# Kernel tuning notes

Measured on AMD Instinct MI355X. Metric: run time of the kernel, lower is better.

## Reference

```python
import jax, jax.numpy as jnp
import numpy as np

B, L, V, H = 64, 2048, 1024, 256
HALF = H // 2


def setup_inputs() -> dict:
    key = jax.random.key(0)
    ks = jax.random.split(key, 8)
    s = lambda k, shape, scale=0.05: jax.random.normal(k, shape, jnp.float32) * scale
    return {
        "seq": jax.random.randint(ks[0], (B, L), 0, V),
        "embed": s(ks[1], (V, H)),
        "w1": s(ks[2], (H, 2 * H)), "b1": jnp.zeros((2 * H,), jnp.float32),
        "w2": s(ks[3], (2 * H, H)), "b2": jnp.zeros((H,), jnp.float32),
        "ln_g": jnp.ones((H,), jnp.float32), "ln_b": jnp.zeros((H,), jnp.float32),
        "kp_w": s(ks[4], (H, H)), "kp_b": jnp.zeros((H,), jnp.float32),
        "out_w": s(ks[5], (H, V)), "out_b": jnp.zeros((V,), jnp.float32),
    }


def _forward(seq, embed, w1, b1, w2, b2, ln_g, ln_b, kp_w, kp_b, out_w, out_b):
    # Encoder: embed -> FFN residual -> LayerNorm
    e = embed[seq]                                    # [B, L, H]
    ff = jax.nn.relu(e @ w1 + b1) @ w2 + b2           # [B, L, H]
    x = e + ff
    mu = x.mean(-1, keepdims=True)
    var = jnp.mean((x - mu) ** 2, -1, keepdims=True)
    h = (x - mu) * jax.lax.rsqrt(var + 1e-5) * ln_g + ln_b

    # Shared key projection for all timesteps at once
    proj = h @ kp_w + kp_b                            # [B, L, H]
    ks_all = proj[:, : L - 1, :HALF]                  # [B, L-1, half]
    ke_all = proj[:, : L - 1, HALF:]                  # [B, L-1, half]
    scale = (jnp.arange(L - 1, dtype=jnp.float32) + 1.0) / L  # (t+1)/L

    def step(carry, inp):
        M_s, M_e = carry
        k_s, k_e, sc = inp                            # [B,half], [B,half], scalar
        vps = jnp.einsum('bij,bj->bi', M_s, k_s)
        dvs = k_s - vps / (jnp.sum(k_s * k_s, -1, keepdims=True) + 1e-6)
        M_s = M_s + jnp.einsum('bi,bj->bij', dvs, k_s)
        vpe = jnp.einsum('bij,bj->bi', M_e, k_e)
        dve = k_e - vpe / (jnp.sum(k_e * k_e, -1, keepdims=True) + 1e-6)
        M_e = M_e + sc * jnp.einsum('bi,bj->bij', dve, k_e)
        return (M_s, M_e), None

    M0 = jnp.zeros((B, HALF, HALF), jnp.float32)
    (M_s, M_e), _ = jax.lax.scan(
        step, (M0, M0),
        (ks_all.transpose(1, 0, 2), ke_all.transpose(1, 0, 2), scale))

    q = proj[:, -1, :]                                # query from last step
    cs = jnp.einsum('bij,bj->bi', M_s, q[:, :HALF])
    ce = jnp.einsum('bij,bj->bi', M_e, q[:, HALF:])
    return jnp.concatenate([cs, ce], -1) @ out_w + out_b  # [B, V]


def reference(seq, embed, w1, b1, w2, b2, ln_g, ln_b, kp_w, kp_b, out_w, out_b):
    return _forward(seq, embed, w1, b1, w2, b2, ln_g, ln_b, kp_w, kp_b, out_w, out_b)
```

## Files before the change

kernel.cpp:

```cpp
#include <hip/hip_runtime.h>
#include <hip/hip_bf16.h>
#include <stdint.h>

#define B_SZ 64
#define L_SZ 2048
#define V_SZ 1024
#define H_SZ 256
#define HALF_SZ 128
#define NTOK (B_SZ * L_SZ)
#define CH 16384

typedef unsigned short ushort_t;
typedef __attribute__((ext_vector_type(8))) short bf16x8;
typedef __attribute__((ext_vector_type(4))) float f32x4;

__device__ __forceinline__ ushort_t f2bf(float f) {
    __hip_bfloat16 h = __float2bfloat16(f);
    return *reinterpret_cast<ushort_t*>(&h);
}

__global__ __launch_bounds__(256) void cvt_bf16_k(
    const float* __restrict__ src, ushort_t* __restrict__ dst, int n)
{
    int i = (blockIdx.x * 256 + threadIdx.x) * 4;
    if (i >= n) return;
    float4 v = *(const float4*)(src + i);
    uint2 pk;
    pk.x = (uint32_t)f2bf(v.x) | ((uint32_t)f2bf(v.y) << 16);
    pk.y = (uint32_t)f2bf(v.z) | ((uint32_t)f2bf(v.w) << 16);
    *(uint2*)(dst + i) = pk;
}

__global__ __launch_bounds__(256) void transpose_cvt_k(
    const float* __restrict__ src, ushort_t* __restrict__ dst, int K, int N)
{
    int idx = blockIdx.x * 256 + threadIdx.x;
    if (idx >= K * N) return;
    int n = idx / K;
    int k = idx - n * K;
    dst[idx] = f2bf(src[(size_t)k * N + n]);
}

template <int MODE, int K, int N>
__global__ __launch_bounds__(256) void gemm_mfma(
    const ushort_t* __restrict__ A, const ushort_t* __restrict__ BT,
    const float* __restrict__ bias, void* __restrict__ Cp,
    const int* __restrict__ seq, const float* __restrict__ embed)
{
    __shared__ __align__(16) ushort_t Asm[128 * 64];
    __shared__ __align__(16) ushort_t Bsm[128 * 64];

    const int tid = threadIdx.x;
    const int m0 = blockIdx.x * 128;
    const int n0 = blockIdx.y * 128;
    const int w = tid >> 6;
    const int l = tid & 63;
    const int wr = w >> 1;
    const int wc = w & 1;

    const ushort_t* arow[4];
    const ushort_t* brow[4];
#pragma unroll
    for (int i = 0; i < 4; ++i) {
        const int flat = i * 256 + tid;
        const int r = flat >> 3;
        const int gr = (MODE == 1) ? seq[m0 + r] : (m0 + r);
        arow[i] = A + (size_t)gr * K;
        brow[i] = BT + (size_t)(n0 + r) * K;
    }

    f32x4 acc[4][4];
#pragma unroll
    for (int mi = 0; mi < 4; ++mi)
#pragma unroll
        for (int nj = 0; nj < 4; ++nj)
            acc[mi][nj] = (f32x4){0.f, 0.f, 0.f, 0.f};

    for (int kt = 0; kt < K / 64; ++kt) {
#pragma unroll
        for (int i = 0; i < 4; ++i) {
            const int flat = i * 256 + tid;
            const int r = flat >> 3;
            const int c = flat & 7;
            const int cs = c ^ (r & 7);
            uint4 av = *(const uint4*)(arow[i] + kt * 64 + c * 8);
            *(uint4*)&Asm[r * 64 + cs * 8] = av;
            uint4 bv = *(const uint4*)(brow[i] + kt * 64 + c * 8);
            *(uint4*)&Bsm[r * 64 + cs * 8] = bv;
        }
        __syncthreads();
#pragma unroll
        for (int kh = 0; kh < 2; ++kh) {
            bf16x8 af[4], bfr[4];
#pragma unroll
            for (int mi = 0; mi < 4; ++mi) {
                const int r = wr * 64 + mi * 16 + (l & 15);
                const int c = (kh * 4 + (l >> 4)) ^ (r & 7);
                af[mi] = *(const bf16x8*)&Asm[r * 64 + c * 8];
            }
#pragma unroll
            for (int nj = 0; nj < 4; ++nj) {
                const int r = wc * 64 + nj * 16 + (l & 15);
                const int c = (kh * 4 + (l >> 4)) ^ (r & 7);
                bfr[nj] = *(const bf16x8*)&Bsm[r * 64 + c * 8];
            }
#pragma unroll
            for (int mi = 0; mi < 4; ++mi)
#pragma unroll
                for (int nj = 0; nj < 4; ++nj)
                    acc[mi][nj] = __builtin_amdgcn_mfma_f32_16x16x32_bf16(
                        af[mi], bfr[nj], acc[mi][nj], 0, 0, 0);
        }
        __syncthreads();
    }

    const int cl = l & 15;
    const int rg = l >> 4;
    float bv[4];
#pragma unroll
    for (int nj = 0; nj < 4; ++nj)
        bv[nj] = bias[n0 + wc * 64 + nj * 16 + cl];

#pragma unroll
    for (int mi = 0; mi < 4; ++mi) {
#pragma unroll
        for (int i = 0; i < 4; ++i) {
            const int row = m0 + wr * 64 + mi * 16 + rg * 4 + i;
            const float* erow = (MODE == 2)
                ? (embed + (size_t)seq[row] * H_SZ) : nullptr;
#pragma unroll
            for (int nj = 0; nj < 4; ++nj) {
                const int gn = n0 + wc * 64 + nj * 16 + cl;
                float v = acc[mi][nj][i] + bv[nj];
                if (MODE == 1) {
                    v = fmaxf(v, 0.f);
                    ((ushort_t*)Cp)[(size_t)row * N + gn] = f2bf(v);
                } else if (MODE == 2) {
                    ((float*)Cp)[(size_t)row * N + gn] = v + erow[gn];
                } else {
                    ((float*)Cp)[(size_t)row * N + gn] = v;
                }
            }
        }
    }
}

__global__ __launch_bounds__(256) void ln_k(
    const float* __restrict__ x, const float* __restrict__ g,
    const float* __restrict__ bt, ushort_t* __restrict__ h)
{
    const int token = blockIdx.x * 4 + (threadIdx.x >> 6);
    const int lane = threadIdx.x & 63;
    const float* xr = x + (size_t)token * H_SZ + lane * 4;
    const float4 v = *(const float4*)xr;
    float s = v.x + v.y + v.z + v.w;
    float sq = v.x * v.x + v.y * v.y + v.z * v.z + v.w * v.w;
#pragma unroll
    for (int m = 1; m < 64; m <<= 1) {
        s += __shfl_xor(s, m);
        sq += __shfl_xor(sq, m);
    }
    const float mu = s * (1.f / H_SZ);
    const float var = sq * (1.f / H_SZ) - mu * mu;
    const float rs = rsqrtf(var + 1e-5f);
    const int idx = lane * 4;
    const float4 gg = *(const float4*)(g + idx);
    const float4 bb = *(const float4*)(bt + idx);
    ushort_t o0 = f2bf((v.x - mu) * rs * gg.x + bb.x);
    ushort_t o1 = f2bf((v.y - mu) * rs * gg.y + bb.y);
    ushort_t o2 = f2bf((v.z - mu) * rs * gg.z + bb.z);
    ushort_t o3 = f2bf((v.w - mu) * rs * gg.w + bb.w);
    uint2 pk;
    pk.x = (uint32_t)o0 | ((uint32_t)o1 << 16);
    pk.y = (uint32_t)o2 | ((uint32_t)o3 << 16);
    *(uint2*)(h + (size_t)token * H_SZ + idx) = pk;
}

__global__ __launch_bounds__(256) void invn_k(
    const float* __restrict__ proj, float* __restrict__ invn)
{
    const int token = blockIdx.x * 4 + (threadIdx.x >> 6);
    const int lane = threadIdx.x & 63;
    const float4 v = *(const float4*)(proj + (size_t)token * H_SZ + lane * 4);
    float sq = v.x * v.x + v.y * v.y + v.z * v.z + v.w * v.w;
#pragma unroll
    for (int m = 1; m < 32; m <<= 1) sq += __shfl_xor(sq, m);
    if ((lane & 31) == 0)
        invn[(size_t)token * 2 + (lane >> 5)] = 1.0f / (sq + 1e-6f);
}

__global__ __launch_bounds__(64) void scan_bw_k(
    const float* __restrict__ proj, const float* __restrict__ invn,
    float* __restrict__ cbuf)
{
    const int pair = blockIdx.x;
    const int b = pair >> 1;
    const int half = pair & 1;
    const int l = threadIdx.x;

    const float* kbase = proj + (size_t)b * L_SZ * H_SZ + half * HALF_SZ;
    const float* ibase = invn + (size_t)b * L_SZ * 2 + half;
    const float invL = 1.0f / (float)L_SZ;

    float2 v = *(const float2*)(kbase + (size_t)(L_SZ - 1) * H_SZ + 2 * l);
    float2 c = make_float2(0.f, 0.f);

    float2 kc[4], kn[4];
    float inc_[4], inn_[4];
#pragma unroll
    for (int i = 0; i < 4; ++i) {
        kc[i] = *(const float2*)(kbase + (size_t)(2046 - i) * H_SZ + 2 * l);
        inc_[i] = ibase[(size_t)(2046 - i) * 2];
        kn[i] = *(const float2*)(kbase + (size_t)(2042 - i) * H_SZ + 2 * l);
        inn_[i] = ibase[(size_t)(2042 - i) * 2];
    }

    for (int tb = 2046; tb >= 6; tb -= 4) {
        float2 kf[4];
        float inf_[4];
#pragma unroll
        for (int i = 0; i < 4; ++i) {
            int tp = tb - 8 - i;
            tp = tp < 0 ? 0 : tp;
            kf[i] = *(const float2*)(kbase + (size_t)tp * H_SZ + 2 * l);
            inf_[i] = ibase[(size_t)tp * 2];
        }

        float r[10];
        r[0] = kc[0].x * v.x + kc[0].y * v.y;
        r[1] = kc[1].x * v.x + kc[1].y * v.y;
        r[2] = kc[2].x * v.x + kc[2].y * v.y;
        r[3] = kc[3].x * v.x + kc[3].y * v.y;
        r[4] = kc[0].x * kc[1].x + kc[0].y * kc[1].y;
        r[5] = kc[0].x * kc[2].x + kc[0].y * kc[2].y;
        r[6] = kc[0].x * kc[3].x + kc[0].y * kc[3].y;
        r[7] = kc[1].x * kc[2].x + kc[1].y * kc[2].y;
        r[8] = kc[1].x * kc[3].x + kc[1].y * kc[3].y;
        r[9] = kc[2].x * kc[3].x + kc[2].y * kc[3].y;

#pragma unroll
        for (int m = 1; m < 64; m <<= 1) {
#pragma unroll
            for (int j = 0; j < 10; ++j) r[j] += __shfl_xor(r[j], m);
        }

        float be[4], al[4];
#pragma unroll
        for (int i = 0; i < 4; ++i) {
            be[i] = half ? (float)(tb - i + 1) * invL : 1.0f;
            al[i] = be[i] * inc_[i];
        }
        const float d0 = r[0];
        const float d1 = r[1] - al[0] * r[4] * d0;
        const float d2 = r[2] - al[0] * r[5] * d0 - al[1] * r[7] * d1;
        const float d3 = r[3] - al[0] * r[6] * d0 - al[1] * r[8] * d1
                              - al[2] * r[9] * d2;

        const float ad0 = al[0] * d0, ad1 = al[1] * d1,
                    ad2 = al[2] * d2, ad3 = al[3] * d3;
        const float bd0 = be[0] * d0, bd1 = be[1] * d1,
                    bd2 = be[2] * d2, bd3 = be[3] * d3;

        v.x -= ad0 * kc[0].x + ad1 * kc[1].x + ad2 * kc[2].x + ad3 * kc[3].x;
        v.y -= ad0 * kc[0].y + ad1 * kc[1].y + ad2 * kc[2].y + ad3 * kc[3].y;
        c.x += bd0 * kc[0].x + bd1 * kc[1].x + bd2 * kc[2].x + bd3 * kc[3].x;
        c.y += bd0 * kc[0].y + bd1 * kc[1].y + bd2 * kc[2].y + bd3 * kc[3].y;

#pragma unroll
        for (int i = 0; i < 4; ++i) {
            kc[i] = kn[i]; inc_[i] = inn_[i];
            kn[i] = kf[i]; inn_[i] = inf_[i];
        }
    }

#pragma unroll
    for (int i = 0; i < 3; ++i) {
        const int t = 2 - i;
        float a = kc[i].x * v.x + kc[i].y * v.y;
#pragma unroll
        for (int m = 1; m < 64; m <<= 1) a += __shfl_xor(a, m);
        const float be = half ? (float)(t + 1) * invL : 1.0f;
        const float al = be * inc_[i];
        const float ad = al * a, bd = be * a;
        v.x -= ad * kc[i].x; v.y -= ad * kc[i].y;
        c.x += bd * kc[i].x; c.y += bd * kc[i].y;
    }

    *(float2*)(cbuf + b * H_SZ + half * HALF_SZ + 2 * l) = c;
}

__global__ __launch_bounds__(256) void out_k(
    const float* __restrict__ c, const float* __restrict__ w,
    const float* __restrict__ ob, float* __restrict__ out)
{
    const int b = blockIdx.x >> 2;
    const int v = ((blockIdx.x & 3) << 8) + threadIdx.x;
    const float* cb = c + b * H_SZ;
    float acc = ob[v];
#pragma unroll 4
    for (int hh = 0; hh < H_SZ; ++hh)
        acc = fmaf(cb[hh], w[(size_t)hh * V_SZ + v], acc);
    out[(size_t)b * V_SZ + v] = acc;
}

extern "C" void kernel_launch(void* const* d_in, const int* in_sizes, int n_in,
                              void* d_out, int out_size, void* d_ws, size_t ws_size,
                              hipStream_t stream)
{
    const int*   seq   = (const int*)d_in[0];
    const float* embed = (const float*)d_in[1];
    const float* w1    = (const float*)d_in[2];
    const float* b1    = (const float*)d_in[3];
    const float* w2    = (const float*)d_in[4];
    const float* b2    = (const float*)d_in[5];
    const float* ln_g  = (const float*)d_in[6];
    const float* ln_b  = (const float*)d_in[7];
    const float* kp_w  = (const float*)d_in[8];
    const float* kp_b  = (const float*)d_in[9];
    const float* out_w = (const float*)d_in[10];
    const float* out_b = (const float*)d_in[11];

    char* ws = (char*)d_ws;
    size_t off = 0;
    auto alloc = [&](size_t bytes) -> void* {
        void* p = ws + off;
        off += (bytes + 255) & ~(size_t)255;
        return p;
    };

    float*    proj = (float*)alloc((size_t)NTOK * H_SZ * sizeof(float));
    ushort_t* t1_c = (ushort_t*)alloc((size_t)CH * 512 * sizeof(ushort_t));
    float*    x_c  = (float*)alloc((size_t)CH * H_SZ * sizeof(float));
    ushort_t* h_c  = (ushort_t*)alloc((size_t)CH * H_SZ * sizeof(ushort_t));
    float*    invn = (float*)alloc((size_t)NTOK * 2 * sizeof(float));
    float*    cbuf = (float*)alloc((size_t)B_SZ * H_SZ * sizeof(float));
    ushort_t* embed_bf = (ushort_t*)alloc((size_t)V_SZ * H_SZ * 2);
    ushort_t* w1T = (ushort_t*)alloc((size_t)512 * 256 * 2);
    ushort_t* w2T = (ushort_t*)alloc((size_t)256 * 512 * 2);
    ushort_t* kpT = (ushort_t*)alloc((size_t)256 * 256 * 2);
    float*    outp = (float*)d_out;

    const dim3 blk(256);

    cvt_bf16_k<<<dim3((V_SZ * H_SZ) / 1024), blk, 0, stream>>>(
        embed, embed_bf, V_SZ * H_SZ);
    transpose_cvt_k<<<dim3((256 * 512) / 256), blk, 0, stream>>>(w1, w1T, 256, 512);
    transpose_cvt_k<<<dim3((512 * 256) / 256), blk, 0, stream>>>(w2, w2T, 512, 256);
    transpose_cvt_k<<<dim3((256 * 256) / 256), blk, 0, stream>>>(kp_w, kpT, 256, 256);

    for (int c = 0; c < NTOK / CH; ++c) {
        const int base = c * CH;
        const int* seq_c = seq + base;
        gemm_mfma<1, 256, 512><<<dim3(CH / 128, 4), blk, 0, stream>>>(
            embed_bf, w1T, b1, t1_c, seq_c, nullptr);
        gemm_mfma<2, 512, 256><<<dim3(CH / 128, 2), blk, 0, stream>>>(
            t1_c, w2T, b2, x_c, seq_c, embed);
        ln_k<<<dim3(CH / 4), blk, 0, stream>>>(x_c, ln_g, ln_b, h_c);
        gemm_mfma<3, 256, 256><<<dim3(CH / 128, 2), blk, 0, stream>>>(
            h_c, kpT, kp_b, proj + (size_t)base * H_SZ, seq_c, nullptr);
    }

    invn_k<<<dim3(NTOK / 4), blk, 0, stream>>>(proj, invn);
    scan_bw_k<<<dim3(128), dim3(64), 0, stream>>>(proj, invn, cbuf);
    out_k<<<dim3(B_SZ * 4), blk, 0, stream>>>(cbuf, out_w, out_b, outp);
}
```

Before: 799.6 us.

## Replace serial backward scan with chunked Gram-matrix solve using split-bf16 MFMA

Replaces the per-step backward scan (one 64-lane wave per batch-half, 4 steps per iteration with shuffle reductions) with a chunked algorithm. Each 128-token chunk goes into LDS as split hi/lo bf16, and a 128x128 Gram matrix is built with three-pass MFMA for near-fp32 accuracy. A triangular forward substitution then produces all per-step coefficients, and v and c are updated in bulk. Key norms are computed in the same kernel, so the separate invn kernel and its buffer are removed. The serial per-token dependency chain shrinks to a 128-step LDS substitution per chunk, at the cost of extra MFMA work, heavy LDS use (about 100KB per block) and only 128 blocks.

```diff
diff --git a/kernel.cpp b/kernel.cpp
--- a/kernel.cpp
+++ b/kernel.cpp
@@ -176,117 +176,193 @@
     *(uint2*)(h + (size_t)token * H_SZ + idx) = pk;
 }
 
-__global__ __launch_bounds__(256) void invn_k(
-    const float* __restrict__ proj, float* __restrict__ invn)
-{
-    const int token = blockIdx.x * 4 + (threadIdx.x >> 6);
-    const int lane = threadIdx.x & 63;
-    const float4 v = *(const float4*)(proj + (size_t)token * H_SZ + lane * 4);
-    float sq = v.x * v.x + v.y * v.y + v.z * v.z + v.w * v.w;
-#pragma unroll
-    for (int m = 1; m < 32; m <<= 1) sq += __shfl_xor(sq, m);
-    if ((lane & 31) == 0)
-        invn[(size_t)token * 2 + (lane >> 5)] = 1.0f / (sq + 1e-6f);
-}
-
-__global__ __launch_bounds__(64) void scan_bw_k(
-    const float* __restrict__ proj, const float* __restrict__ invn,
-    float* __restrict__ cbuf)
-{
+__global__ __launch_bounds__(256) void scan_chunk_k(
+    const float* __restrict__ proj, float* __restrict__ cbuf)
+{
+    __shared__ __align__(16) ushort_t Khi[128 * 128];
+    __shared__ __align__(16) ushort_t Klo[128 * 128];
+    __shared__ __align__(16) float G[128 * 128];
+    __shared__ float vv[128], cc[128], aa[128];
+    __shared__ float al[128], be[128], ad[128], bd[128];
+    __shared__ float pv[2][128], pc[2][128];
+
     const int pair = blockIdx.x;
     const int b = pair >> 1;
     const int half = pair & 1;
-    const int l = threadIdx.x;
+    const int tid = threadIdx.x;
+    const int w = tid >> 6;
+    const int l = tid & 63;
 
     const float* kbase = proj + (size_t)b * L_SZ * H_SZ + half * HALF_SZ;
-    const float* ibase = invn + (size_t)b * L_SZ * 2 + half;
     const float invL = 1.0f / (float)L_SZ;
 
-    float2 v = *(const float2*)(kbase + (size_t)(L_SZ - 1) * H_SZ + 2 * l);
-    float2 c = make_float2(0.f, 0.f);
-
-    float2 kc[4], kn[4];
-    float inc_[4], inn_[4];
-#pragma unroll
-    for (int i = 0; i < 4; ++i) {
-        kc[i] = *(const float2*)(kbase + (size_t)(2046 - i) * H_SZ + 2 * l);
-        inc_[i] = ibase[(size_t)(2046 - i) * 2];
-        kn[i] = *(const float2*)(kbase + (size_t)(2042 - i) * H_SZ + 2 * l);
-        inn_[i] = ibase[(size_t)(2042 - i) * 2];
-    }
-
-    for (int tb = 2046; tb >= 6; tb -= 4) {
-        float2 kf[4];
-        float inf_[4];
-#pragma unroll
-        for (int i = 0; i < 4; ++i) {
-            int tp = tb - 8 - i;
-            tp = tp < 0 ? 0 : tp;
-            kf[i] = *(const float2*)(kbase + (size_t)tp * H_SZ + 2 * l);
-            inf_[i] = ibase[(size_t)tp * 2];
-        }
-
-        float r[10];
-        r[0] = kc[0].x * v.x + kc[0].y * v.y;
-        r[1] = kc[1].x * v.x + kc[1].y * v.y;
-        r[2] = kc[2].x * v.x + kc[2].y * v.y;
-        r[3] = kc[3].x * v.x + kc[3].y * v.y;
-        r[4] = kc[0].x * kc[1].x + kc[0].y * kc[1].y;
-        r[5] = kc[0].x * kc[2].x + kc[0].y * kc[2].y;
-        r[6] = kc[0].x * kc[3].x + kc[0].y * kc[3].y;
-        r[7] = kc[1].x * kc[2].x + kc[1].y * kc[2].y;
-        r[8] = kc[1].x * kc[3].x + kc[1].y * kc[3].y;
-        r[9] = kc[2].x * kc[3].x + kc[2].y * kc[3].y;
-
-#pragma unroll
-        for (int m = 1; m < 64; m <<= 1) {
-#pragma unroll
-            for (int j = 0; j < 10; ++j) r[j] += __shfl_xor(r[j], m);
-        }
-
-        float be[4], al[4];
-#pragma unroll
-        for (int i = 0; i < 4; ++i) {
-            be[i] = half ? (float)(tb - i + 1) * invL : 1.0f;
-            al[i] = be[i] * inc_[i];
-        }
-        const float d0 = r[0];
-        const float d1 = r[1] - al[0] * r[4] * d0;
-        const float d2 = r[2] - al[0] * r[5] * d0 - al[1] * r[7] * d1;
-        const float d3 = r[3] - al[0] * r[6] * d0 - al[1] * r[8] * d1
-                              - al[2] * r[9] * d2;
-
-        const float ad0 = al[0] * d0, ad1 = al[1] * d1,
-                    ad2 = al[2] * d2, ad3 = al[3] * d3;
-        const float bd0 = be[0] * d0, bd1 = be[1] * d1,
-                    bd2 = be[2] * d2, bd3 = be[3] * d3;
-
-        v.x -= ad0 * kc[0].x + ad1 * kc[1].x + ad2 * kc[2].x + ad3 * kc[3].x;
-        v.y -= ad0 * kc[0].y + ad1 * kc[1].y + ad2 * kc[2].y + ad3 * kc[3].y;
-        c.x += bd0 * kc[0].x + bd1 * kc[1].x + bd2 * kc[2].x + bd3 * kc[3].x;
-        c.y += bd0 * kc[0].y + bd1 * kc[1].y + bd2 * kc[2].y + bd3 * kc[3].y;
-
-#pragma unroll
-        for (int i = 0; i < 4; ++i) {
-            kc[i] = kn[i]; inc_[i] = inn_[i];
-            kn[i] = kf[i]; inn_[i] = inf_[i];
-        }
-    }
-
-#pragma unroll
-    for (int i = 0; i < 3; ++i) {
-        const int t = 2 - i;
-        float a = kc[i].x * v.x + kc[i].y * v.y;
-#pragma unroll
-        for (int m = 1; m < 64; m <<= 1) a += __shfl_xor(a, m);
-        const float be = half ? (float)(t + 1) * invL : 1.0f;
-        const float al = be * inc_[i];
-        const float ad = al * a, bd = be * a;
-        v.x -= ad * kc[i].x; v.y -= ad * kc[i].y;
-        c.x += bd * kc[i].x; c.y += bd * kc[i].y;
-    }
-
-    *(float2*)(cbuf + b * H_SZ + half * HALF_SZ + 2 * l) = c;
+    if (tid < 128) {
+        vv[tid] = kbase[(size_t)(L_SZ - 1) * H_SZ + tid];
+        cc[tid] = 0.f;
+    }
+    __syncthreads();
+
+    for (int chk = 15; chk >= 0; --chk) {
+        const int t1 = chk * 128 + 127;
+
+        {
+            const int u = tid >> 1, h = tid & 1;
+            const int tok = t1 - u;
+            const float* src = kbase + (size_t)tok * H_SZ + h * 64;
+            float sq = 0.f;
+#pragma unroll
+            for (int g = 0; g < 8; ++g) {
+                const float4 v0 = *(const float4*)(src + g * 8);
+                const float4 v1 = *(const float4*)(src + g * 8 + 4);
+                const float e[8] = {v0.x, v0.y, v0.z, v0.w,
+                                    v1.x, v1.y, v1.z, v1.w};
+                ushort_t hi8[8], lo8[8];
+#pragma unroll
+                for (int q = 0; q < 8; ++q) {
+                    sq = fmaf(e[q], e[q], sq);
+                    hi8[q] = f2bf(e[q]);
+                    const float hf = __uint_as_float(((uint32_t)hi8[q]) << 16);
+                    lo8[q] = f2bf(e[q] - hf);
+                }
+                const int cs = (h * 8 + g) ^ (u & 7);
+                uint4 ph, pl;
+                ph.x = (uint32_t)hi8[0] | ((uint32_t)hi8[1] << 16);
+                ph.y = (uint32_t)hi8[2] | ((uint32_t)hi8[3] << 16);
+                ph.z = (uint32_t)hi8[4] | ((uint32_t)hi8[5] << 16);
+                ph.w = (uint32_t)hi8[6] | ((uint32_t)hi8[7] << 16);
+                pl.x = (uint32_t)lo8[0] | ((uint32_t)lo8[1] << 16);
+                pl.y = (uint32_t)lo8[2] | ((uint32_t)lo8[3] << 16);
+                pl.z = (uint32_t)lo8[4] | ((uint32_t)lo8[5] << 16);
+                pl.w = (uint32_t)lo8[6] | ((uint32_t)lo8[7] << 16);
+                *(uint4*)&Khi[u * 128 + cs * 8] = ph;
+                *(uint4*)&Klo[u * 128 + cs * 8] = pl;
+            }
+            sq += __shfl_xor(sq, 1);
+            if (h == 0) {
+                float bet, alp;
+                if (tok == L_SZ - 1) { bet = 0.f; alp = 0.f; }
+                else {
+                    bet = half ? (float)(tok + 1) * invL : 1.0f;
+                    alp = bet / (sq + 1e-6f);
+                }
+                al[u] = alp; be[u] = bet;
+            }
+        }
+        __syncthreads();
+
+        {
+#pragma unroll
+            for (int tr = 0; tr < 2; ++tr) {
+                const int ti = 2 * w + tr;
+                const int ra = ti * 16 + (l & 15);
+                bf16x8 ahi[4], alo[4];
+#pragma unroll
+                for (int ks = 0; ks < 4; ++ks) {
+                    const int c = (ks * 4 + (l >> 4)) ^ (ra & 7);
+                    ahi[ks] = *(const bf16x8*)&Khi[ra * 128 + c * 8];
+                    alo[ks] = *(const bf16x8*)&Klo[ra * 128 + c * 8];
+                }
+#pragma unroll
+                for (int tj = 0; tj < 8; ++tj) {
+                    const int rb = tj * 16 + (l & 15);
+                    f32x4 acc = (f32x4){0.f, 0.f, 0.f, 0.f};
+#pragma unroll
+                    for (int ks = 0; ks < 4; ++ks) {
+                        const int c = (ks * 4 + (l >> 4)) ^ (rb & 7);
+                        const bf16x8 bhi = *(const bf16x8*)&Khi[rb * 128 + c * 8];
+                        const bf16x8 blo = *(const bf16x8*)&Klo[rb * 128 + c * 8];
+                        acc = __builtin_amdgcn_mfma_f32_16x16x32_bf16(
+                            ahi[ks], bhi, acc, 0, 0, 0);
+                        acc = __builtin_amdgcn_mfma_f32_16x16x32_bf16(
+                            ahi[ks], blo, acc, 0, 0, 0);
+                        acc = __builtin_amdgcn_mfma_f32_16x16x32_bf16(
+                            alo[ks], bhi, acc, 0, 0, 0);
+                    }
+                    const int col = tj * 16 + (l & 15);
+                    const int rbase = ti * 16 + (l >> 4) * 4;
+#pragma unroll
+                    for (int i = 0; i < 4; ++i)
+                        G[(rbase + i) * 128 + col] = acc[i];
+                }
+            }
+        }
+
+        {
+            const int u = tid >> 1, h = tid & 1;
+            float p = 0.f;
+#pragma unroll
+            for (int g = 0; g < 8; ++g) {
+                const int cs = (h * 8 + g) ^ (u & 7);
+                const uint4 ph = *(const uint4*)&Khi[u * 128 + cs * 8];
+                const uint4 pl = *(const uint4*)&Klo[u * 128 + cs * 8];
+                const float* vp = &vv[(h * 8 + g) * 8];
+                const float4 w0 = *(const float4*)vp;
+                const float4 w1 = *(const float4*)(vp + 4);
+                const uint32_t Hh[4] = {ph.x, ph.y, ph.z, ph.w};
+                const uint32_t Ll[4] = {pl.x, pl.y, pl.z, pl.w};
+                const float wv[8] = {w0.x, w0.y, w0.z, w0.w,
+                                     w1.x, w1.y, w1.z, w1.w};
+#pragma unroll
+                for (int q = 0; q < 4; ++q) {
+                    const float k0 = __uint_as_float(Hh[q] << 16)
+                                   + __uint_as_float(Ll[q] << 16);
+                    const float k1 = __uint_as_float(Hh[q] & 0xffff0000u)
+                                   + __uint_as_float(Ll[q] & 0xffff0000u);
+                    p = fmaf(k0, wv[2 * q], p);
+                    p = fmaf(k1, wv[2 * q + 1], p);
+                }
+            }
+            p += __shfl_xor(p, 1);
+            if (h == 0) aa[u] = p;
+        }
+        __syncthreads();
+
+        {
+            float acc0 = aa[l];
+            float acc1 = aa[l + 64];
+#pragma unroll 8
+            for (int j = 0; j < 128; ++j) {
+                const float cur = (j < 64) ? acc0 : acc1;
+                const float db = __shfl(cur, j & 63);
+                const float adj = al[j] * db;
+                const float g0 = G[j * 128 + l];
+                const float g1 = G[j * 128 + l + 64];
+                acc0 -= ((l > j) ? adj : 0.f) * g0;
+                acc1 -= ((l + 64 > j) ? adj : 0.f) * g1;
+                if (w == 0 && l == (j & 63)) {
+                    ad[j] = adj;
+                    bd[j] = be[j] * db;
+                }
+            }
+        }
+        __syncthreads();
+
+        {
+            const int g = tid >> 7;
+            const int e = tid & 127;
+            const int ch0 = e >> 3, o = e & 7;
+            float pvv = 0.f, pcc = 0.f;
+#pragma unroll 8
+            for (int j = g * 64; j < g * 64 + 64; ++j) {
+                const int idx = j * 128 + ((ch0 ^ (j & 7)) << 3) + o;
+                const float k = __uint_as_float(((uint32_t)Khi[idx]) << 16)
+                              + __uint_as_float(((uint32_t)Klo[idx]) << 16);
+                pvv = fmaf(ad[j], k, pvv);
+                pcc = fmaf(bd[j], k, pcc);
+            }
+            pv[g][e] = pvv; pc[g][e] = pcc;
+        }
+        __syncthreads();
+
+        if (tid < 128) {
+            vv[tid] -= pv[0][tid] + pv[1][tid];
+            cc[tid] += pc[0][tid] + pc[1][tid];
+        }
+        __syncthreads();
+    }
+
+    if (tid < 128)
+        cbuf[b * H_SZ + half * HALF_SZ + tid] = cc[tid];
 }
 
 __global__ __launch_bounds__(256) void out_k(
@@ -332,7 +408,6 @@
     ushort_t* t1_c = (ushort_t*)alloc((size_t)CH * 512 * sizeof(ushort_t));
     float*    x_c  = (float*)alloc((size_t)CH * H_SZ * sizeof(float));
     ushort_t* h_c  = (ushort_t*)alloc((size_t)CH * H_SZ * sizeof(ushort_t));
-    float*    invn = (float*)alloc((size_t)NTOK * 2 * sizeof(float));
     float*    cbuf = (float*)alloc((size_t)B_SZ * H_SZ * sizeof(float));
     ushort_t* embed_bf = (ushort_t*)alloc((size_t)V_SZ * H_SZ * 2);
     ushort_t* w1T = (ushort_t*)alloc((size_t)512 * 256 * 2);
@@ -360,7 +435,6 @@
             h_c, kpT, kp_b, proj + (size_t)base * H_SZ, seq_c, nullptr);
     }
 
-    invn_k<<<dim3(NTOK / 4), blk, 0, stream>>>(proj, invn);
-    scan_bw_k<<<dim3(128), dim3(64), 0, stream>>>(proj, invn, cbuf);
+    scan_chunk_k<<<dim3(128), blk, 0, stream>>>(proj, cbuf);
     out_k<<<dim3(B_SZ * 4), blk, 0, stream>>>(cbuf, out_w, out_b, outp);
 }
```

Measured after the change: 824.8 us. +3.1%, slower.

## Precompute blocked Gram coefficients in parallel; scan backward in blocks of eight

Applied to the files above, without the earlier changes.

Moves the key-key Gram products and inverse-norm scaling out of the sequential backward scan into a parallel pre-pass that writes per-block coefficient sets of eight tokens. The scan then does only eight query dot products per step with one batched wave reduction and a small triangular solve, halving the number of serial steps. This cuts reductions on the latency-bound critical path of the 128-wave scan, at the cost of an extra kernel, a coefficient buffer, and higher register pressure in the scan.

```diff
diff --git a/kernel.cpp b/kernel.cpp
--- a/kernel.cpp
+++ b/kernel.cpp
@@ -176,21 +176,68 @@
     *(uint2*)(h + (size_t)token * H_SZ + idx) = pk;
 }
 
-__global__ __launch_bounds__(256) void invn_k(
-    const float* __restrict__ proj, float* __restrict__ invn)
-{
-    const int token = blockIdx.x * 4 + (threadIdx.x >> 6);
-    const int lane = threadIdx.x & 63;
-    const float4 v = *(const float4*)(proj + (size_t)token * H_SZ + lane * 4);
-    float sq = v.x * v.x + v.y * v.y + v.z * v.z + v.w * v.w;
-#pragma unroll
-    for (int m = 1; m < 32; m <<= 1) sq += __shfl_xor(sq, m);
-    if ((lane & 31) == 0)
-        invn[(size_t)token * 2 + (lane >> 5)] = 1.0f / (sq + 1e-6f);
-}
-
-__global__ __launch_bounds__(64) void scan_bw_k(
-    const float* __restrict__ proj, const float* __restrict__ invn,
+__global__ __launch_bounds__(256) void gram8_k(
+    const float* __restrict__ proj, float* __restrict__ g8)
+{
+    const int pair = blockIdx.y;
+    const int b = pair >> 1;
+    const int half = pair & 1;
+    const int bi = blockIdx.x * 4 + (threadIdx.x >> 6);
+    const int l = threadIdx.x & 63;
+
+    const float* kbase = proj + (size_t)b * L_SZ * H_SZ + half * HALF_SZ;
+
+    float2 kk[8];
+#pragma unroll
+    for (int i = 0; i < 8; ++i) {
+        const int tok = bi * 8 + 7 - i;
+        kk[i] = *(const float2*)(kbase + (size_t)tok * H_SZ + 2 * l);
+    }
+
+    float r[36];
+#pragma unroll
+    for (int i = 0; i < 8; ++i)
+        r[i] = kk[i].x * kk[i].x + kk[i].y * kk[i].y;
+#pragma unroll
+    for (int i = 1; i < 8; ++i)
+#pragma unroll
+        for (int j = 0; j < i; ++j)
+            r[8 + i * (i - 1) / 2 + j] = kk[i].x * kk[j].x + kk[i].y * kk[j].y;
+
+#pragma unroll
+    for (int m = 1; m < 64; m <<= 1)
+#pragma unroll
+        for (int t = 0; t < 36; ++t)
+            r[t] += __shfl_xor(r[t], m);
+
+    const float invL = 1.0f / (float)L_SZ;
+    float al[8], be[8];
+#pragma unroll
+    for (int i = 0; i < 8; ++i) {
+        const int tok = bi * 8 + 7 - i;
+        const float bet = (tok == L_SZ - 1)
+            ? 0.f : (half ? (float)(tok + 1) * invL : 1.0f);
+        be[i] = bet;
+        al[i] = bet / (r[i] + 1e-6f);
+    }
+
+    if (l == 0) {
+        float* out = g8 + ((size_t)pair * 256 + bi) * 48;
+#pragma unroll
+        for (int i = 1; i < 8; ++i)
+#pragma unroll
+            for (int j = 0; j < i; ++j)
+                out[i * (i - 1) / 2 + j] = al[j] * r[8 + i * (i - 1) / 2 + j];
+#pragma unroll
+        for (int i = 0; i < 8; ++i) {
+            out[28 + i] = al[i];
+            out[36 + i] = be[i];
+        }
+    }
+}
+
+__global__ __launch_bounds__(64) void scan_bw8_k(
+    const float* __restrict__ proj, const float* __restrict__ g8,
     float* __restrict__ cbuf)
 {
     const int pair = blockIdx.x;
@@ -199,91 +246,77 @@
     const int l = threadIdx.x;
 
     const float* kbase = proj + (size_t)b * L_SZ * H_SZ + half * HALF_SZ;
-    const float* ibase = invn + (size_t)b * L_SZ * 2 + half;
-    const float invL = 1.0f / (float)L_SZ;
+    const float* gbase = g8 + (size_t)pair * 256 * 48;
 
     float2 v = *(const float2*)(kbase + (size_t)(L_SZ - 1) * H_SZ + 2 * l);
     float2 c = make_float2(0.f, 0.f);
 
-    float2 kc[4], kn[4];
-    float inc_[4], inn_[4];
-#pragma unroll
-    for (int i = 0; i < 4; ++i) {
-        kc[i] = *(const float2*)(kbase + (size_t)(2046 - i) * H_SZ + 2 * l);
-        inc_[i] = ibase[(size_t)(2046 - i) * 2];
-        kn[i] = *(const float2*)(kbase + (size_t)(2042 - i) * H_SZ + 2 * l);
-        inn_[i] = ibase[(size_t)(2042 - i) * 2];
-    }
-
-    for (int tb = 2046; tb >= 6; tb -= 4) {
-        float2 kf[4];
-        float inf_[4];
-#pragma unroll
-        for (int i = 0; i < 4; ++i) {
-            int tp = tb - 8 - i;
-            tp = tp < 0 ? 0 : tp;
-            kf[i] = *(const float2*)(kbase + (size_t)tp * H_SZ + 2 * l);
-            inf_[i] = ibase[(size_t)tp * 2];
-        }
-
-        float r[10];
-        r[0] = kc[0].x * v.x + kc[0].y * v.y;
-        r[1] = kc[1].x * v.x + kc[1].y * v.y;
-        r[2] = kc[2].x * v.x + kc[2].y * v.y;
-        r[3] = kc[3].x * v.x + kc[3].y * v.y;
-        r[4] = kc[0].x * kc[1].x + kc[0].y * kc[1].y;
-        r[5] = kc[0].x * kc[2].x + kc[0].y * kc[2].y;
-        r[6] = kc[0].x * kc[3].x + kc[0].y * kc[3].y;
-        r[7] = kc[1].x * kc[2].x + kc[1].y * kc[2].y;
-        r[8] = kc[1].x * kc[3].x + kc[1].y * kc[3].y;
-        r[9] = kc[2].x * kc[3].x + kc[2].y * kc[3].y;
-
-#pragma unroll
-        for (int m = 1; m < 64; m <<= 1) {
-#pragma unroll
-            for (int j = 0; j < 10; ++j) r[j] += __shfl_xor(r[j], m);
-        }
-
-        float be[4], al[4];
-#pragma unroll
-        for (int i = 0; i < 4; ++i) {
-            be[i] = half ? (float)(tb - i + 1) * invL : 1.0f;
-            al[i] = be[i] * inc_[i];
-        }
-        const float d0 = r[0];
-        const float d1 = r[1] - al[0] * r[4] * d0;
-        const float d2 = r[2] - al[0] * r[5] * d0 - al[1] * r[7] * d1;
-        const float d3 = r[3] - al[0] * r[6] * d0 - al[1] * r[8] * d1
-                              - al[2] * r[9] * d2;
-
-        const float ad0 = al[0] * d0, ad1 = al[1] * d1,
-                    ad2 = al[2] * d2, ad3 = al[3] * d3;
-        const float bd0 = be[0] * d0, bd1 = be[1] * d1,
-                    bd2 = be[2] * d2, bd3 = be[3] * d3;
-
-        v.x -= ad0 * kc[0].x + ad1 * kc[1].x + ad2 * kc[2].x + ad3 * kc[3].x;
-        v.y -= ad0 * kc[0].y + ad1 * kc[1].y + ad2 * kc[2].y + ad3 * kc[3].y;
-        c.x += bd0 * kc[0].x + bd1 * kc[1].x + bd2 * kc[2].x + bd3 * kc[3].x;
-        c.y += bd0 * kc[0].y + bd1 * kc[1].y + bd2 * kc[2].y + bd3 * kc[3].y;
-
-#pragma unroll
-        for (int i = 0; i < 4; ++i) {
-            kc[i] = kn[i]; inc_[i] = inn_[i];
-            kn[i] = kf[i]; inn_[i] = inf_[i];
-        }
-    }
-
-#pragma unroll
-    for (int i = 0; i < 3; ++i) {
-        const int t = 2 - i;
-        float a = kc[i].x * v.x + kc[i].y * v.y;
-#pragma unroll
-        for (int m = 1; m < 64; m <<= 1) a += __shfl_xor(a, m);
-        const float be = half ? (float)(t + 1) * invL : 1.0f;
-        const float al = be * inc_[i];
-        const float ad = al * a, bd = be * a;
-        v.x -= ad * kc[i].x; v.y -= ad * kc[i].y;
-        c.x += bd * kc[i].x; c.y += bd * kc[i].y;
+    float2 kc[8], kn[8], kf[8];
+    float Gc[48], Gf[48];
+
+#pragma unroll
+    for (int i = 0; i < 8; ++i) {
+        kc[i] = *(const float2*)(kbase + (size_t)(255 * 8 + 7 - i) * H_SZ + 2 * l);
+        kn[i] = *(const float2*)(kbase + (size_t)(254 * 8 + 7 - i) * H_SZ + 2 * l);
+    }
+    {
+        const float4* gp = (const float4*)(gbase + (size_t)255 * 48);
+#pragma unroll
+        for (int i = 0; i < 12; ++i) *(float4*)(Gc + 4 * i) = gp[i];
+    }
+
+    for (int bi = 255; bi >= 0; --bi) {
+        const int kp = (bi >= 2) ? bi - 2 : 0;
+        const int gp_ = (bi >= 1) ? bi - 1 : 0;
+#pragma unroll
+        for (int i = 0; i < 8; ++i)
+            kf[i] = *(const float2*)(kbase + (size_t)(kp * 8 + 7 - i) * H_SZ + 2 * l);
+        {
+            const float4* gp2 = (const float4*)(gbase + (size_t)gp_ * 48);
+#pragma unroll
+            for (int i = 0; i < 12; ++i) *(float4*)(Gf + 4 * i) = gp2[i];
+        }
+
+        float a[8];
+#pragma unroll
+        for (int i = 0; i < 8; ++i)
+            a[i] = kc[i].x * v.x + kc[i].y * v.y;
+#pragma unroll
+        for (int m = 1; m < 64; m <<= 1)
+#pragma unroll
+            for (int i = 0; i < 8; ++i)
+                a[i] += __shfl_xor(a[i], m);
+
+        float d[8];
+#pragma unroll
+        for (int i = 0; i < 8; ++i) {
+            float t = a[i];
+            const int off = i * (i - 1) / 2;
+#pragma unroll
+            for (int j = 0; j < i; ++j)
+                t -= Gc[off + j] * d[j];
+            d[i] = t;
+        }
+
+        float ad[8], bd[8];
+#pragma unroll
+        for (int i = 0; i < 8; ++i) {
+            ad[i] = Gc[28 + i] * d[i];
+            bd[i] = Gc[36 + i] * d[i];
+        }
+
+#pragma unroll
+        for (int i = 0; i < 8; ++i) {
+            v.x = fmaf(-ad[i], kc[i].x, v.x);
+            v.y = fmaf(-ad[i], kc[i].y, v.y);
+            c.x = fmaf(bd[i], kc[i].x, c.x);
+            c.y = fmaf(bd[i], kc[i].y, c.y);
+        }
+
+#pragma unroll
+        for (int i = 0; i < 8; ++i) { kc[i] = kn[i]; kn[i] = kf[i]; }
+#pragma unroll
+        for (int j = 0; j < 48; ++j) Gc[j] = Gf[j];
     }
 
     *(float2*)(cbuf + b * H_SZ + half * HALF_SZ + 2 * l) = c;
@@ -332,7 +365,7 @@
     ushort_t* t1_c = (ushort_t*)alloc((size_t)CH * 512 * sizeof(ushort_t));
     float*    x_c  = (float*)alloc((size_t)CH * H_SZ * sizeof(float));
     ushort_t* h_c  = (ushort_t*)alloc((size_t)CH * H_SZ * sizeof(ushort_t));
-    float*    invn = (float*)alloc((size_t)NTOK * 2 * sizeof(float));
+    float*    g8   = (float*)alloc((size_t)128 * 256 * 48 * sizeof(float));
     float*    cbuf = (float*)alloc((size_t)B_SZ * H_SZ * sizeof(float));
     ushort_t* embed_bf = (ushort_t*)alloc((size_t)V_SZ * H_SZ * 2);
     ushort_t* w1T = (ushort_t*)alloc((size_t)512 * 256 * 2);
@@ -360,7 +393,7 @@
             h_c, kpT, kp_b, proj + (size_t)base * H_SZ, seq_c, nullptr);
     }
 
-    invn_k<<<dim3(NTOK / 4), blk, 0, stream>>>(proj, invn);
-    scan_bw_k<<<dim3(128), dim3(64), 0, stream>>>(proj, invn, cbuf);
+    gram8_k<<<dim3(64, 128), blk, 0, stream>>>(proj, g8);
+    scan_bw8_k<<<dim3(128), dim3(64), 0, stream>>>(proj, g8, cbuf);
     out_k<<<dim3(B_SZ * 4), blk, 0, stream>>>(cbuf, out_w, out_b, outp);
 }
```

After: 911.6 us. 1.14x slower.
